# Kernel tuning notes

Hardware: AMD Instinct MI355X
Metric: run time of the kernel (lower is better)

Reference implementation:

```python
import jax, jax.numpy as jnp
import numpy as np

B, T, C = 4, 2048, 1024
H = 16
D = C // H  # 64


def setup_inputs() -> dict:
    key = jax.random.key(0)
    k1, k2, k3 = jax.random.split(key, 3)
    x = jax.random.normal(k1, (B, T, C), dtype=jnp.float32)
    w_qkv = jax.random.normal(k2, (C, 3 * C), dtype=jnp.float32) * (C ** -0.5)
    b_qkv = jnp.zeros((3 * C,), dtype=jnp.float32)
    w_proj = jax.random.normal(k3, (C, C), dtype=jnp.float32) * (C ** -0.5)
    b_proj = jnp.zeros((C,), dtype=jnp.float32)
    return {"x": x, "w_qkv": w_qkv, "b_qkv": b_qkv, "w_proj": w_proj, "b_proj": b_proj}


def reference(x, w_qkv, b_qkv, w_proj, b_proj):
    qkv = x @ w_qkv + b_qkv                      # [B,T,3C]
    q, k, v = jnp.split(qkv, 3, axis=-1)
    # [B,T,C] -> [B,H,T,D]
    q = q.reshape(B, T, H, D).transpose(0, 2, 1, 3)
    k = k.reshape(B, T, H, D).transpose(0, 2, 1, 3)
    v = v.reshape(B, T, H, D).transpose(0, 2, 1, 3)
    scale = 1.0 / jnp.sqrt(jnp.float32(D))
    att = jnp.einsum('bhqd,bhkd->bhqk', q, k) * scale  # [B,H,T,T]
    causal = jnp.tril(jnp.ones((T, T), dtype=bool))
    att = jnp.where(causal[None, None], att, -jnp.inf)
    att = jax.nn.softmax(att, axis=-1)
    y = jnp.einsum('bhqk,bhkd->bhqd', att, v)          # [B,H,T,D]
    y = y.transpose(0, 2, 1, 3).reshape(B, T, C)
    return y @ w_proj + b_proj
```

## Files before the change

kernel.cpp:

```cpp
#include <hip/hip_runtime.h>
#include <hip/hip_bf16.h>
#include <stdint.h>

#define B_ 4
#define T_ 2048
#define C_ 1024
#define H_ 16
#define D_ 64

typedef __bf16 bf16;
typedef _Float16 f16;
typedef __attribute__((ext_vector_type(8))) __bf16 bf16x8;
typedef __attribute__((ext_vector_type(4))) __bf16 bf16x4;
typedef __attribute__((ext_vector_type(4))) _Float16 f16x4;
typedef __attribute__((ext_vector_type(8))) _Float16 f16x8;
typedef __attribute__((ext_vector_type(4))) float floatx4;

__device__ __forceinline__ floatx4 mfma16(bf16x8 a, bf16x8 b, floatx4 c) {
  return __builtin_amdgcn_mfma_f32_16x16x32_bf16(a, b, c, 0, 0, 0);
}
__device__ __forceinline__ floatx4 mfma_pv(f16x4 a, f16x4 b, floatx4 c) {
  return __builtin_amdgcn_mfma_f32_16x16x16f16(a, b, c, 0, 0, 0);
}

__device__ __forceinline__ void gl_lds16(const void* g, void* l) {
  __builtin_amdgcn_global_load_lds(
      (__attribute__((address_space(1))) uint32_t*)g,
      (__attribute__((address_space(3))) uint32_t*)l, 16, 0, 0);
}

__global__ __launch_bounds__(256) void cvt_bf16(const float* __restrict__ in,
                                                bf16* __restrict__ out) {
  const size_t i = ((size_t)blockIdx.x * 256 + threadIdx.x) * 4;
  const floatx4 v = *(const floatx4*)(in + i);
  bf16x4 r;
#pragma unroll
  for (int j = 0; j < 4; j++) r[j] = (bf16)v[j];
  *(bf16x4*)(out + i) = r;
}

__global__ __launch_bounds__(256) void transpose_f32(const float* __restrict__ in,
                                                     bf16* __restrict__ out,
                                                     int K, int N) {
  __shared__ bf16 tile[32][33];
  const int n0 = blockIdx.x * 32, k0 = blockIdx.y * 32;
  const int r = threadIdx.x >> 5, c = threadIdx.x & 31;
#pragma unroll
  for (int i = 0; i < 4; i++)
    tile[r + i * 8][c] = (bf16)in[(size_t)(k0 + r + i * 8) * N + n0 + c];
  __syncthreads();
#pragma unroll
  for (int i = 0; i < 4; i++)
    out[(size_t)(n0 + r + i * 8) * K + k0 + c] = tile[c][r + i * 8];
}

template <int MODE>
__global__ __launch_bounds__(256) void gemm128(const bf16* __restrict__ A,
                                               const bf16* __restrict__ Bt,
                                               const float* __restrict__ bias,
                                               void* __restrict__ o0,
                                               bf16* __restrict__ o1,
                                               f16* __restrict__ o2,
                                               int M, int N, int K) {
  __shared__ __align__(16) bf16 As[128 * 32];
  __shared__ __align__(16) bf16 Bs[128 * 32];
  const int tid = threadIdx.x;
  const int m0 = blockIdx.y * 128, n0 = blockIdx.x * 128;
  const int lane = tid & 63, wv = tid >> 6;
  const int wm = (wv >> 1) * 64, wn = (wv & 1) * 64;
  const int col = lane & 15, quad = lane >> 4;

  floatx4 acc[4][4];
#pragma unroll
  for (int i = 0; i < 4; i++)
#pragma unroll
    for (int j = 0; j < 4; j++) acc[i][j] = (floatx4){0.f, 0.f, 0.f, 0.f};

  const int c0 = tid, c1 = tid + 256;
  const bf16* a0 = A + (size_t)(m0 + (c0 >> 2)) * K + (c0 & 3) * 8;
  const bf16* a1 = A + (size_t)(m0 + (c1 >> 2)) * K + (c1 & 3) * 8;
  const bf16* b0 = Bt + (size_t)(n0 + (c0 >> 2)) * K + (c0 & 3) * 8;
  const bf16* b1 = Bt + (size_t)(n0 + (c1 >> 2)) * K + (c1 & 3) * 8;
  bf16* lA0 = &As[(wv * 64) * 8];
  bf16* lA1 = &As[(wv * 64 + 256) * 8];
  bf16* lB0 = &Bs[(wv * 64) * 8];
  bf16* lB1 = &Bs[(wv * 64 + 256) * 8];

  for (int kt = 0; kt < K; kt += 32) {
    gl_lds16(a0 + kt, lA0);
    gl_lds16(a1 + kt, lA1);
    gl_lds16(b0 + kt, lB0);
    gl_lds16(b1 + kt, lB1);
    __syncthreads();
    bf16x8 afr[4], bg[4];
#pragma unroll
    for (int mb = 0; mb < 4; mb++)
      afr[mb] = *(const bf16x8*)&As[(wm + mb * 16 + col) * 32 + quad * 8];
#pragma unroll
    for (int nb = 0; nb < 4; nb++)
      bg[nb] = *(const bf16x8*)&Bs[(wn + nb * 16 + col) * 32 + quad * 8];
#pragma unroll
    for (int mb = 0; mb < 4; mb++)
#pragma unroll
      for (int nb = 0; nb < 4; nb++)
        acc[mb][nb] = mfma16(afr[mb], bg[nb], acc[mb][nb]);
    __syncthreads();
  }

#pragma unroll
  for (int mb = 0; mb < 4; mb++) {
    const int mg = m0 + wm + mb * 16 + quad * 4;
#pragma unroll
    for (int nb = 0; nb < 4; nb++) {
      const int ng = n0 + wn + nb * 16 + col;
      const float bs = bias[ng];
      if (MODE == 0) {
        const int third = ng >> 10;
        const int nn = ng & 1023;
        const int h = nn >> 6, d = nn & 63;
#pragma unroll
        for (int r = 0; r < 4; r++) {
          const int mm = mg + r;
          const int bb = mm >> 11, t = mm & 2047;
          const float v = acc[mb][nb][r] + bs;
          const size_t bh = (size_t)bb * H_ + h;
          if (third == 0) {
            ((bf16*)o0)[(bh * T_ + t) * D_ + d] = (bf16)v;
          } else if (third == 1) {
            const int lane2 = (t & 15) | (((d >> 3) & 3) << 4);
            const size_t idx =
                ((((bh * 64 + (t >> 5)) * 2 + ((t >> 4) & 1)) * 2 + (d >> 5)) * 64 +
                 lane2) * 8 + (d & 7);
            o1[idx] = (bf16)v;
          } else {
            const int lane2 = (d & 15) | (((t >> 2) & 3) << 4);
            const size_t idx =
                (((bh * 64 + (t >> 5)) * 4 + (d >> 4)) * 64 + lane2) * 8 +
                ((t >> 4) & 1) * 4 + (t & 3);
            o2[idx] = (f16)v;
          }
        }
      } else {
#pragma unroll
        for (int r = 0; r < 4; r++)
          ((float*)o0)[(size_t)(mg + r) * N + ng] = acc[mb][nb][r] + bs;
      }
    }
  }
}

__global__ __launch_bounds__(256, 4) void attn(const bf16* __restrict__ Q,
                                               const bf16* __restrict__ Kp,
                                               const f16* __restrict__ Vp,
                                               bf16* __restrict__ Y) {
  const int tid = threadIdx.x, lane = tid & 63, wv = tid >> 6;
  const int col = lane & 15, quad = lane >> 4;
  const int id = blockIdx.x;
  const int j = id >> 3;
  const int bh = ((j & 7) << 3) | (id & 7);
  const int qtile = 63 - (j >> 3);
  const int b = bh >> 4, h = bh & 15;
  const int qbase = qtile * 32;

  __shared__ __align__(16) floatx4 mbuf[3][8][64];
  __shared__ float lbuf[3][2][64];

  bf16x8 qf[2][2];
#pragma unroll
  for (int mq = 0; mq < 2; mq++) {
    const bf16* qp = Q + ((size_t)bh * T_ + qbase + mq * 16 + col) * D_ + quad * 8;
    qf[mq][0] = *(const bf16x8*)qp;
    qf[mq][1] = *(const bf16x8*)(qp + 32);
  }

  floatx4 o[2][4];
  float lsum[2] = {0.f, 0.f};
#pragma unroll
  for (int mq = 0; mq < 2; mq++)
#pragma unroll
    for (int s = 0; s < 4; s++) o[mq][s] = (floatx4){0.f, 0.f, 0.f, 0.f};

  const float C1 = 0.18033688f;
  const float C2 = 11.541560f;

  const int nmine = (qtile >= wv) ? ((qtile - wv) >> 2) + 1 : 0;

  for (int i = 0; i < nmine; i++) {
    const int kt = wv + 4 * i;
    const bool masked = (kt == qtile);
    const bf16* kbase = Kp + ((size_t)bh * 64 + kt) * 2048 + lane * 8;
    const f16* vbase = Vp + ((size_t)bh * 64 + kt) * 2048 + lane * 8;
    bf16x8 ka[2][2];
    ka[0][0] = *(const bf16x8*)(kbase);
    ka[0][1] = *(const bf16x8*)(kbase + 512);
    ka[1][0] = *(const bf16x8*)(kbase + 1024);
    ka[1][1] = *(const bf16x8*)(kbase + 1536);
    f16x8 vv[4];
#pragma unroll
    for (int sub = 0; sub < 4; sub++) vv[sub] = *(const f16x8*)(vbase + sub * 512);

#pragma unroll
    for (int st = 0; st < 2; st++) {
#pragma unroll
      for (int mq = 0; mq < 2; mq++) {
        if (masked && mq == 0 && st == 1) continue;
        floatx4 s = (floatx4){0.f, 0.f, 0.f, 0.f};
        s = mfma16(ka[st][0], qf[mq][0], s);
        s = mfma16(ka[st][1], qf[mq][1], s);
        f16x4 pf;
        float ps = 0.f;
        const bool diag = masked && (mq == st);
#pragma unroll
        for (int r = 0; r < 4; r++) {
          float p = exp2f(fmaf(s[r], C1, -C2));
          if (diag && (quad * 4 + r > col)) p = 0.f;
          ps += p;
          pf[r] = (f16)p;
        }
        lsum[mq] += ps;
#pragma unroll
        for (int sub = 0; sub < 4; sub++) {
          f16x4 va;
#pragma unroll
          for (int jj = 0; jj < 4; jj++) va[jj] = vv[sub][st * 4 + jj];
          o[mq][sub] = mfma_pv(va, pf, o[mq][sub]);
        }
      }
    }
  }

  if (wv != 0) {
#pragma unroll
    for (int mq = 0; mq < 2; mq++) {
#pragma unroll
      for (int sub = 0; sub < 4; sub++) mbuf[wv - 1][mq * 4 + sub][lane] = o[mq][sub];
      lbuf[wv - 1][mq][lane] = lsum[mq];
    }
  }
  __syncthreads();
  if (wv == 0) {
#pragma unroll
    for (int w = 0; w < 3; w++)
#pragma unroll
      for (int mq = 0; mq < 2; mq++) {
#pragma unroll
        for (int sub = 0; sub < 4; sub++) o[mq][sub] += mbuf[w][mq * 4 + sub][lane];
        lsum[mq] += lbuf[w][mq][lane];
      }
#pragma unroll
    for (int mq = 0; mq < 2; mq++) {
      lsum[mq] += __shfl_xor(lsum[mq], 16);
      lsum[mq] += __shfl_xor(lsum[mq], 32);
      const float rinv = 1.f / lsum[mq];
      const int qrow = qbase + mq * 16 + col;
#pragma unroll
      for (int sub = 0; sub < 4; sub++) {
        bf16x4 yv;
#pragma unroll
        for (int r = 0; r < 4; r++) yv[r] = (bf16)(o[mq][sub][r] * rinv);
        *(bf16x4*)&Y[((size_t)b * T_ + qrow) * C_ + h * 64 + sub * 16 + quad * 4] = yv;
      }
    }
  }
}

extern "C" void kernel_launch(void* const* d_in, const int* in_sizes, int n_in,
                              void* d_out, int out_size, void* d_ws, size_t ws_size,
                              hipStream_t stream) {
  (void)in_sizes; (void)n_in; (void)out_size; (void)ws_size;
  const float* x      = (const float*)d_in[0];
  const float* w_qkv  = (const float*)d_in[1];
  const float* b_qkv  = (const float*)d_in[2];
  const float* w_proj = (const float*)d_in[3];
  const float* b_proj = (const float*)d_in[4];

  char* ws = (char*)d_ws;
  bf16* wqkv_t  = (bf16*)(ws);
  bf16* wproj_t = (bf16*)(ws + 6291456);
  bf16* qb      = (bf16*)(ws + 8388608);
  bf16* kbuf    = (bf16*)(ws + 25165824);
  f16*  vtbuf   = (f16*)(ws + 41943040);
  bf16* yb      = (bf16*)(ws + 58720256);
  bf16* xb      = (bf16*)(ws + 58720256);

  cvt_bf16<<<8192, 256, 0, stream>>>(x, xb);
  transpose_f32<<<dim3(96, 32), 256, 0, stream>>>(w_qkv, wqkv_t, 1024, 3072);
  transpose_f32<<<dim3(32, 32), 256, 0, stream>>>(w_proj, wproj_t, 1024, 1024);
  gemm128<0><<<dim3(24, 64), 256, 0, stream>>>(xb, wqkv_t, b_qkv, qb, kbuf, vtbuf,
                                               8192, 3072, 1024);
  attn<<<dim3(4096), 256, 0, stream>>>(qb, kbuf, vtbuf, yb);
  gemm128<1><<<dim3(8, 64), 256, 0, stream>>>(yb, wproj_t, b_proj, d_out, nullptr,
                                              nullptr, 8192, 1024, 1024);
}
```

Baseline: 271.9 us.

## Swap QKV GEMM operands for vectorized epilogue stores and load two K-slices per barrier

The QKV projection GEMM now computes the transposed product (weights as the M operand, tokens as N). Each lane's four accumulator rows therefore map to four consecutive head-dim elements, so the Q and K epilogue can write packed bf16x4 stores instead of scalar ones. The main loop also loads two 32-wide K slices into separate LDS buffers per iteration, which halves the number of barriers. This doubles LDS use per block, and the V path still uses scalar stores.

```diff
diff --git a/kernel.cpp b/kernel.cpp
--- a/kernel.cpp
+++ b/kernel.cpp
@@ -62,8 +62,8 @@
                                                bf16* __restrict__ o1,
                                                f16* __restrict__ o2,
                                                int M, int N, int K) {
-  __shared__ __align__(16) bf16 As[128 * 32];
-  __shared__ __align__(16) bf16 Bs[128 * 32];
+  __shared__ __align__(16) bf16 As[2][128 * 32];
+  __shared__ __align__(16) bf16 Bs[2][128 * 32];
   const int tid = threadIdx.x;
   const int m0 = blockIdx.y * 128, n0 = blockIdx.x * 128;
   const int lane = tid & 63, wv = tid >> 6;
@@ -81,69 +81,87 @@
   const bf16* a1 = A + (size_t)(m0 + (c1 >> 2)) * K + (c1 & 3) * 8;
   const bf16* b0 = Bt + (size_t)(n0 + (c0 >> 2)) * K + (c0 & 3) * 8;
   const bf16* b1 = Bt + (size_t)(n0 + (c1 >> 2)) * K + (c1 & 3) * 8;
-  bf16* lA0 = &As[(wv * 64) * 8];
-  bf16* lA1 = &As[(wv * 64 + 256) * 8];
-  bf16* lB0 = &Bs[(wv * 64) * 8];
-  bf16* lB1 = &Bs[(wv * 64 + 256) * 8];
-
-  for (int kt = 0; kt < K; kt += 32) {
-    gl_lds16(a0 + kt, lA0);
-    gl_lds16(a1 + kt, lA1);
-    gl_lds16(b0 + kt, lB0);
-    gl_lds16(b1 + kt, lB1);
+
+  for (int kt = 0; kt < K; kt += 64) {
+#pragma unroll
+    for (int hf = 0; hf < 2; hf++) {
+      const int ko = kt + hf * 32;
+      gl_lds16(a0 + ko, &As[hf][(wv * 64) * 8]);
+      gl_lds16(a1 + ko, &As[hf][(wv * 64 + 256) * 8]);
+      gl_lds16(b0 + ko, &Bs[hf][(wv * 64) * 8]);
+      gl_lds16(b1 + ko, &Bs[hf][(wv * 64 + 256) * 8]);
+    }
     __syncthreads();
-    bf16x8 afr[4], bg[4];
-#pragma unroll
-    for (int mb = 0; mb < 4; mb++)
-      afr[mb] = *(const bf16x8*)&As[(wm + mb * 16 + col) * 32 + quad * 8];
-#pragma unroll
-    for (int nb = 0; nb < 4; nb++)
-      bg[nb] = *(const bf16x8*)&Bs[(wn + nb * 16 + col) * 32 + quad * 8];
-#pragma unroll
-    for (int mb = 0; mb < 4; mb++)
+#pragma unroll
+    for (int hf = 0; hf < 2; hf++) {
+      bf16x8 afr[4], bg[4];
+#pragma unroll
+      for (int mb = 0; mb < 4; mb++)
+        afr[mb] = *(const bf16x8*)&As[hf][(wm + mb * 16 + col) * 32 + quad * 8];
 #pragma unroll
       for (int nb = 0; nb < 4; nb++)
-        acc[mb][nb] = mfma16(afr[mb], bg[nb], acc[mb][nb]);
+        bg[nb] = *(const bf16x8*)&Bs[hf][(wn + nb * 16 + col) * 32 + quad * 8];
+#pragma unroll
+      for (int mb = 0; mb < 4; mb++)
+#pragma unroll
+        for (int nb = 0; nb < 4; nb++)
+          acc[mb][nb] = mfma16(afr[mb], bg[nb], acc[mb][nb]);
+    }
     __syncthreads();
   }
 
 #pragma unroll
   for (int mb = 0; mb < 4; mb++) {
-    const int mg = m0 + wm + mb * 16 + quad * 4;
-#pragma unroll
-    for (int nb = 0; nb < 4; nb++) {
-      const int ng = n0 + wn + nb * 16 + col;
-      const float bs = bias[ng];
-      if (MODE == 0) {
-        const int third = ng >> 10;
-        const int nn = ng & 1023;
-        const int h = nn >> 6, d = nn & 63;
-#pragma unroll
-        for (int r = 0; r < 4; r++) {
-          const int mm = mg + r;
-          const int bb = mm >> 11, t = mm & 2047;
-          const float v = acc[mb][nb][r] + bs;
-          const size_t bh = (size_t)bb * H_ + h;
-          if (third == 0) {
-            ((bf16*)o0)[(bh * T_ + t) * D_ + d] = (bf16)v;
-          } else if (third == 1) {
-            const int lane2 = (t & 15) | (((d >> 3) & 3) << 4);
+    const int mgq = m0 + wm + mb * 16 + quad * 4;
+    if (MODE == 0) {
+      const int third = mgq >> 10;
+      const int nn0 = mgq & 1023;
+      const int h = nn0 >> 6, d0 = nn0 & 63;
+      float bs[4];
+#pragma unroll
+      for (int r = 0; r < 4; r++) bs[r] = bias[mgq + r];
+#pragma unroll
+      for (int nb = 0; nb < 4; nb++) {
+        const int t = n0 + wn + nb * 16 + col;
+        const int bb = t >> 11, tt = t & 2047;
+        const size_t bh = (size_t)bb * H_ + h;
+        float v[4];
+#pragma unroll
+        for (int r = 0; r < 4; r++) v[r] = acc[mb][nb][r] + bs[r];
+        if (third == 0) {
+          bf16x4 y;
+#pragma unroll
+          for (int r = 0; r < 4; r++) y[r] = (bf16)v[r];
+          *(bf16x4*)&((bf16*)o0)[(bh * T_ + tt) * D_ + d0] = y;
+        } else if (third == 1) {
+          const int lane2 = (tt & 15) | (((d0 >> 3) & 3) << 4);
+          const size_t idx =
+              ((((bh * 64 + (tt >> 5)) * 2 + ((tt >> 4) & 1)) * 2 + (d0 >> 5)) * 64 +
+               lane2) * 8 + (d0 & 7);
+          bf16x4 y;
+#pragma unroll
+          for (int r = 0; r < 4; r++) y[r] = (bf16)v[r];
+          *(bf16x4*)&o1[idx] = y;
+        } else {
+#pragma unroll
+          for (int r = 0; r < 4; r++) {
+            const int d = d0 + r;
+            const int lane2 = (d & 15) | (((tt >> 2) & 3) << 4);
             const size_t idx =
-                ((((bh * 64 + (t >> 5)) * 2 + ((t >> 4) & 1)) * 2 + (d >> 5)) * 64 +
-                 lane2) * 8 + (d & 7);
-            o1[idx] = (bf16)v;
-          } else {
-            const int lane2 = (d & 15) | (((t >> 2) & 3) << 4);
-            const size_t idx =
-                (((bh * 64 + (t >> 5)) * 4 + (d >> 4)) * 64 + lane2) * 8 +
-                ((t >> 4) & 1) * 4 + (t & 3);
-            o2[idx] = (f16)v;
+                (((bh * 64 + (tt >> 5)) * 4 + (d >> 4)) * 64 + lane2) * 8 +
+                ((tt >> 4) & 1) * 4 + (tt & 3);
+            o2[idx] = (f16)v[r];
           }
         }
-      } else {
+      }
+    } else {
+#pragma unroll
+      for (int nb = 0; nb < 4; nb++) {
+        const int ng = n0 + wn + nb * 16 + col;
+        const float bsc = bias[ng];
 #pragma unroll
         for (int r = 0; r < 4; r++)
-          ((float*)o0)[(size_t)(mg + r) * N + ng] = acc[mb][nb][r] + bs;
+          ((float*)o0)[(size_t)(mgq + r) * N + ng] = acc[mb][nb][r] + bsc;
       }
     }
   }
@@ -286,8 +304,8 @@
   cvt_bf16<<<8192, 256, 0, stream>>>(x, xb);
   transpose_f32<<<dim3(96, 32), 256, 0, stream>>>(w_qkv, wqkv_t, 1024, 3072);
   transpose_f32<<<dim3(32, 32), 256, 0, stream>>>(w_proj, wproj_t, 1024, 1024);
-  gemm128<0><<<dim3(24, 64), 256, 0, stream>>>(xb, wqkv_t, b_qkv, qb, kbuf, vtbuf,
-                                               8192, 3072, 1024);
+  gemm128<0><<<dim3(64, 24), 256, 0, stream>>>(wqkv_t, xb, b_qkv, qb, kbuf, vtbuf,
+                                               3072, 8192, 1024);
   attn<<<dim3(4096), 256, 0, stream>>>(qb, kbuf, vtbuf, yb);
   gemm128<1><<<dim3(8, 64), 256, 0, stream>>>(yb, wproj_t, b_proj, d_out, nullptr,
                                               nullptr, 8192, 1024, 1024);
```

After: 258.2 us. -5.0%, faster.
